# Kernel optimization log

Hardware: AMD Instinct MI355X
Metric: run time of the kernel (lower is better)

The kernel has to match this reference:

```python
import jax, jax.numpy as jnp
import numpy as np

B, S, D, H = 256, 128, 1024, 8
DH = D // H  # per-head dim = input_length / head


def setup_inputs() -> dict:
    key = jax.random.key(0)
    ks = jax.random.split(key, 12)
    code = jax.random.normal(ks[0], (B, S, D), dtype=jnp.float32)
    # 0/1 adjacency (PDG relation mask)
    input_relation = jax.random.bernoulli(ks[1], 0.2, (B, S, S)).astype(jnp.float32)
    w = 0.02
    Wq = jax.random.normal(ks[2], (H, D, DH), dtype=jnp.float32) * w
    bq = jnp.zeros((H, DH), dtype=jnp.float32)
    Wk = jax.random.normal(ks[3], (H, D, DH), dtype=jnp.float32) * w
    bk = jnp.zeros((H, DH), dtype=jnp.float32)
    Wv = jax.random.normal(ks[4], (H, D, DH), dtype=jnp.float32) * w
    bv = jnp.zeros((H, DH), dtype=jnp.float32)
    Wo = jax.random.normal(ks[5], (2 * D, D), dtype=jnp.float32) * w
    bo = jnp.zeros((D,), dtype=jnp.float32)
    return {"code": code, "input_relation": input_relation,
            "Wq": Wq, "bq": bq, "Wk": Wk, "bk": bk,
            "Wv": Wv, "bv": bv, "Wo": Wo, "bo": bo}


def reference(code, input_relation, Wq, bq, Wk, bk, Wv, bv, Wo, bo):
    Hn = Wq.shape[0]
    half = Hn // 2
    Sn = code.shape[1]
    E = jnp.eye(Sn, dtype=code.dtype)
    # Faithful to the TF loop: head i < H/2 sees relation + i*I (the loop
    # reassigns input_relation = this_relation + I each iteration);
    # heads i >= H/2 see the ORIGINAL transposed relation.
    i_idx = jnp.arange(half, dtype=code.dtype)  # [half]
    rel_fwd = input_relation[None] + i_idx[:, None, None, None] * E  # [half,B,S,S]
    rel_t = jnp.swapaxes(input_relation, 1, 2)
    rel_bwd = jnp.broadcast_to(rel_t[None], (Hn - half,) + rel_t.shape)
    rels = jnp.concatenate([rel_fwd, rel_bwd], axis=0)  # [H,B,S,S]

    relu = jax.nn.relu
    Q = relu(jnp.einsum('bsd,hdf->hbsf', code, Wq) + bq[:, None, None, :])
    K = relu(jnp.einsum('bsd,hdf->hbsf', code, Wk) + bk[:, None, None, :])
    V = relu(jnp.einsum('bsd,hdf->hbsf', code, Wv) + bv[:, None, None, :])

    attn = jnp.einsum('hbsf,hbtf->hbst', Q, K)  # [H,B,S,S]
    pdg = rels * attn + 1e-11
    # tf.reduce_sum axis=1 (rows) -> our axis=2; axis=2 (cols) -> our axis=3
    indeg = jnp.sqrt(jnp.sum(pdg, axis=2, keepdims=True))   # [H,B,1,S]
    outdeg = jnp.sqrt(jnp.sum(pdg, axis=3, keepdims=True))  # [H,B,S,1]
    pdg = pdg / indeg / outdeg
    softed = rels * pdg
    res = jnp.einsum('hbst,hbtf->hbsf', softed, V)  # [H,B,S,DH]

    # concat heads along features (head 0 first), then concat original code
    all_ch = jnp.transpose(res, (1, 2, 0, 3)).reshape(code.shape[0], Sn, -1)
    add_ori = jnp.concatenate([all_ch, code], axis=-1)  # [B,S,2D]
    out = relu(add_ori @ Wo + bo)
    return out
```

## Files before the change

kernel.cpp:

```cpp
#include <hip/hip_runtime.h>
#include <cstdint>
#include <cstddef>

#define B_  256
#define S_  128
#define D_  1024
#define H_  8
#define DH_ 128
#define M_  (B_ * S_)

typedef _Float16 half8 __attribute__((ext_vector_type(8)));
typedef float    f32x4 __attribute__((ext_vector_type(4)));

#define GLOAD_LDS16(gp, lp)                                                    \
    __builtin_amdgcn_global_load_lds(                                          \
        (const __attribute__((address_space(1))) void*)(gp),                   \
        (__attribute__((address_space(3))) void*)(lp), 16, 0, 0)

__global__ __launch_bounds__(256)
void cvt_code(const float* __restrict__ src, _Float16* __restrict__ dst, int n8)
{
    int i = blockIdx.x * 256 + threadIdx.x;
    if (i >= n8) return;
    const float4* s = (const float4*)src;
    float4 a = s[2 * i], b = s[2 * i + 1];
    half8 o;
    o[0] = (_Float16)a.x; o[1] = (_Float16)a.y; o[2] = (_Float16)a.z; o[3] = (_Float16)a.w;
    o[4] = (_Float16)b.x; o[5] = (_Float16)b.y; o[6] = (_Float16)b.z; o[7] = (_Float16)b.w;
    *(half8*)(dst + (size_t)i * 8) = o;
}

__global__ __launch_bounds__(256)
void cvt_wqkv(const float* __restrict__ Wq, const float* __restrict__ Wk,
              const float* __restrict__ Wv,
              const float* __restrict__ bq, const float* __restrict__ bk,
              const float* __restrict__ bv,
              _Float16* __restrict__ Wt, float* __restrict__ bias_all)
{
    int idx = blockIdx.x * 256 + threadIdx.x;
    if (idx >= 3072 * 128) return;
    int n = idx >> 7, kc = idx & 127, k = kc * 8;
    int qkv = n >> 10, hf = n & 1023, h = hf >> 7, f = hf & 127;
    const float* W = (qkv == 0 ? Wq : (qkv == 1 ? Wk : Wv))
                     + (size_t)h * D_ * DH_ + (size_t)k * DH_ + f;
    half8 o;
    #pragma unroll
    for (int j = 0; j < 8; ++j) o[j] = (_Float16)W[(size_t)j * DH_];
    *(half8*)(Wt + (size_t)n * 1024 + k) = o;
    if (kc == 0)
        bias_all[n] = (qkv == 0 ? bq : (qkv == 1 ? bk : bv))[h * DH_ + f];
}

__global__ __launch_bounds__(256)
void cvt_wo(const float* __restrict__ Wo, _Float16* __restrict__ Wot)
{
    int idx = blockIdx.x * 256 + threadIdx.x;
    if (idx >= 1024 * 256) return;
    int n = idx >> 8, kc = idx & 255, k = kc * 8;
    const float* W = Wo + (size_t)k * 1024 + n;
    half8 o;
    #pragma unroll
    for (int j = 0; j < 8; ++j) o[j] = (_Float16)W[(size_t)j * 1024];
    *(half8*)(Wot + (size_t)n * 2048 + k) = o;
}

template <bool OUTF32>
__global__ __launch_bounds__(512, 4)
void gemm_f16_b32(const _Float16* __restrict__ A1p, const _Float16* __restrict__ A2p,
                  int K1, const _Float16* __restrict__ Bt,
                  const float* __restrict__ bias, void* __restrict__ outp,
                  int Ntot, int Ktot, int ntn)
{
    __shared__ __align__(16) char lds[49152];

    const int tid = threadIdx.x;
    const int w = tid >> 6, l = tid & 63;
    const int wm = w >> 2, wn = w & 3;
    const int lr = l & 15, lg = l >> 4;

    const int cpx = gridDim.x >> 3;
    const int bid = blockIdx.x;
    const int swz = (bid & 7) * cpx + (bid >> 3);
    const int m0 = (swz / ntn) * 128, n0 = (swz % ntn) * 256;

    const int NT = Ktot >> 5;

    auto stage = [&](int bufi, int t) {
        const int k0 = t << 5;
        char* base = lds + bufi * 24576;
        const int rr = l >> 2, cc = (l & 3) * 8;
        {
            const _Float16* Asrc; int kc;
            if (k0 < K1) { Asrc = A1p; kc = k0; } else { Asrc = A2p; kc = k0 - K1; }
            const _Float16* g = Asrc + (size_t)(m0 + w * 16 + rr) * 1024 + kc + cc;
            GLOAD_LDS16(g, base + w * 1024);
        }
        #pragma unroll
        for (int i = 0; i < 2; ++i) {
            const int row = i * 128 + w * 16 + rr;
            const _Float16* g = Bt + (size_t)(n0 + row) * Ktot + k0 + cc;
            GLOAD_LDS16(g, base + 8192 + i * 8192 + w * 1024);
        }
    };

    f32x4 acc[4][4] = {};

    stage(0, 0);

    for (int t = 0; t < NT; ++t) {
        const int buf = t & 1;
        const bool nl = (t + 1 < NT);

        asm volatile("s_waitcnt vmcnt(0)" ::: "memory");
        __builtin_amdgcn_s_barrier();

        if (nl) stage(buf ^ 1, t + 1);

        half8 af[4], bf[4];
        #pragma unroll
        for (int i = 0; i < 4; ++i)
            af[i] = *(const half8*)(lds + buf * 24576 + (wm * 64 + i * 16 + lr) * 64 + lg * 16);
        #pragma unroll
        for (int j = 0; j < 4; ++j)
            bf[j] = *(const half8*)(lds + buf * 24576 + 8192 + (wn * 64 + j * 16 + lr) * 64 + lg * 16);

        __builtin_amdgcn_s_setprio(1);
        #pragma unroll
        for (int i = 0; i < 4; ++i)
            #pragma unroll
            for (int j = 0; j < 4; ++j)
                acc[i][j] = __builtin_amdgcn_mfma_f32_16x16x32_f16(
                    af[i], bf[j], acc[i][j], 0, 0, 0);
        __builtin_amdgcn_s_setprio(0);
    }

    #pragma unroll
    for (int i = 0; i < 4; ++i) {
        #pragma unroll
        for (int j = 0; j < 4; ++j) {
            const int n = n0 + wn * 64 + j * 16 + lr;
            const float bs = bias[n];
            #pragma unroll
            for (int rg = 0; rg < 4; ++rg) {
                const int m = m0 + wm * 64 + i * 16 + lg * 4 + rg;
                float v = acc[i][j][rg] + bs;
                v = v > 0.0f ? v : 0.0f;
                if constexpr (OUTF32)
                    ((float*)outp)[(size_t)m * Ntot + n] = v;
                else
                    ((_Float16*)outp)[(size_t)m * Ntot + n] = (_Float16)v;
            }
        }
    }
}

__global__ __launch_bounds__(256, 2)
void attn_pdg_mfma(const _Float16* __restrict__ QKV, const float* __restrict__ Rel,
                   _Float16* __restrict__ resh)
{
    __shared__ __align__(16) char smem[75776];
    unsigned* rbits = (unsigned*)(smem + 70656);
    float* rowpart  = (float*)(smem + 72704);
    float* colpart  = (float*)(smem + 73728);
    float* inv_in   = (float*)(smem + 74752);
    float* inv_out  = (float*)(smem + 75264);

    const int tid = threadIdx.x;
    const int w = tid >> 6, l = tid & 63;
    const int wr = w >> 1, wc = w & 1;
    const int lr = l & 15, lg = l >> 4;
    const int h = blockIdx.x, b = blockIdx.y;

    for (int s = w; s < S_; s += 4) {
        const float* row = &Rel[((size_t)b * S_ + s) * S_];
        unsigned long long b0m = __ballot(row[l] > 0.5f);
        unsigned long long b1m = __ballot(row[64 + l] > 0.5f);
        if (l == 0) {
            rbits[s * 4 + 0] = (unsigned)b0m; rbits[s * 4 + 1] = (unsigned)(b0m >> 32);
            rbits[s * 4 + 2] = (unsigned)b1m; rbits[s * 4 + 3] = (unsigned)(b1m >> 32);
        }
    }

    const size_t gbase = (size_t)(b * S_) * 3072 + h * DH_;

    const _Float16* Vb = QKV + gbase + 2048;
    const int vrow = tid >> 1, vcol0 = (tid & 1) * 64;
    uint4 vreg[8];
    #pragma unroll
    for (int j = 0; j < 8; ++j)
        vreg[j] = *(const uint4*)&Vb[(size_t)vrow * 3072 + vcol0 + j * 8];

    #pragma unroll
    for (int i = 0; i < 8; ++i) {
        const int row = (w * 8 + i) * 4 + (l >> 4);
        const int gsrc = (l & 15) ^ (row & 7);
        const _Float16* gq = QKV + gbase + (size_t)row * 3072 + gsrc * 8;
        GLOAD_LDS16(gq, smem + (w * 8 + i) * 1024);
        const _Float16* gk = QKV + gbase + 1024 + (size_t)row * 3072 + gsrc * 8;
        GLOAD_LDS16(gk, smem + 32768 + (w * 8 + i) * 1024);
    }
    __syncthreads();

    f32x4 acc[4][4] = {};
    #pragma unroll
    for (int kc = 0; kc < 4; ++kc) {
        half8 af[4], bf[4];
        #pragma unroll
        for (int i = 0; i < 4; ++i) {
            const int row = wr * 64 + i * 16 + lr;
            const int pos = (kc * 4 + lg) ^ (row & 7);
            af[i] = *(const half8*)(smem + row * 256 + pos * 16);
        }
        #pragma unroll
        for (int j = 0; j < 4; ++j) {
            const int row = wc * 64 + j * 16 + lr;
            const int pos = (kc * 4 + lg) ^ (row & 7);
            bf[j] = *(const half8*)(smem + 32768 + row * 256 + pos * 16);
        }
        #pragma unroll
        for (int i = 0; i < 4; ++i)
            #pragma unroll
            for (int j = 0; j < 4; ++j)
                acc[i][j] = __builtin_amdgcn_mfma_f32_16x16x32_f16(af[i], bf[j], acc[i][j], 0, 0, 0);
    }

    auto relf = [&](int s, int t) -> float {
        float r;
        if (h < H_ / 2) {
            r = (float)((rbits[s * 4 + (t >> 5)] >> (t & 31)) & 1u);
            if (s == t) r += (float)h;
        } else {
            r = (float)((rbits[t * 4 + (s >> 5)] >> (s & 31)) & 1u);
        }
        return r;
    };

    f32x4 p[4][4];
    #pragma unroll
    for (int i = 0; i < 4; ++i)
        #pragma unroll
        for (int j = 0; j < 4; ++j)
            #pragma unroll
            for (int rg = 0; rg < 4; ++rg) {
                const int s = wr * 64 + i * 16 + lg * 4 + rg;
                const int t = wc * 64 + j * 16 + lr;
                p[i][j][rg] = relf(s, t) * acc[i][j][rg] + 1e-11f;
            }

    #pragma unroll
    for (int i = 0; i < 4; ++i)
        #pragma unroll
        for (int rg = 0; rg < 4; ++rg) {
            float part = p[i][0][rg] + p[i][1][rg] + p[i][2][rg] + p[i][3][rg];
            part += __shfl_xor(part, 1);
            part += __shfl_xor(part, 2);
            part += __shfl_xor(part, 4);
            part += __shfl_xor(part, 8);
            if (lr == 0) rowpart[wc * 128 + wr * 64 + i * 16 + lg * 4 + rg] = part;
        }
    #pragma unroll
    for (int j = 0; j < 4; ++j) {
        float part = 0.0f;
        #pragma unroll
        for (int i = 0; i < 4; ++i)
            part += p[i][j][0] + p[i][j][1] + p[i][j][2] + p[i][j][3];
        part += __shfl_xor(part, 16);
        part += __shfl_xor(part, 32);
        if (lg == 0) colpart[wr * 128 + wc * 64 + j * 16 + lr] = part;
    }
    __syncthreads();

    if (tid < 128) {
        inv_in[tid] = rsqrtf(colpart[tid] + colpart[128 + tid]);
    } else {
        const int s = tid - 128;
        inv_out[s] = rsqrtf(rowpart[s] + rowpart[128 + s]);
    }
    __syncthreads();

    float itj[4];
    #pragma unroll
    for (int j = 0; j < 4; ++j) itj[j] = inv_in[wc * 64 + j * 16 + lr];
    #pragma unroll
    for (int i = 0; i < 4; ++i)
        #pragma unroll
        for (int rg = 0; rg < 4; ++rg) {
            const int s = wr * 64 + i * 16 + lg * 4 + rg;
            const float os = inv_out[s];
            #pragma unroll
            for (int j = 0; j < 4; ++j) {
                const int t = wc * 64 + j * 16 + lr;
                const float val = relf(s, t) * p[i][j][rg] * itj[j] * os;
                *(_Float16*)(smem + s * 272 + t * 2) = (_Float16)val;
            }
        }

    #pragma unroll
    for (int j = 0; j < 8; ++j) {
        union { uint4 u; _Float16 hh[8]; } uu;
        uu.u = vreg[j];
        #pragma unroll
        for (int e = 0; e < 8; ++e) {
            const int f = vcol0 + j * 8 + e;
            *(_Float16*)(smem + 34816 + f * 280 + vrow * 2) = uu.hh[e];
        }
    }
    __syncthreads();

    f32x4 acc2[4][4] = {};
    #pragma unroll
    for (int kc = 0; kc < 4; ++kc) {
        half8 af[4], bf[4];
        #pragma unroll
        for (int i = 0; i < 4; ++i)
            af[i] = *(const half8*)(smem + (wr * 64 + i * 16 + lr) * 272 + kc * 64 + lg * 16);
        #pragma unroll
        for (int j = 0; j < 4; ++j)
            bf[j] = *(const half8*)(smem + 34816 + (wc * 64 + j * 16 + lr) * 280 + kc * 64 + lg * 16);
        #pragma unroll
        for (int i = 0; i < 4; ++i)
            #pragma unroll
            for (int j = 0; j < 4; ++j)
                acc2[i][j] = __builtin_amdgcn_mfma_f32_16x16x32_f16(af[i], bf[j], acc2[i][j], 0, 0, 0);
    }

    #pragma unroll
    for (int i = 0; i < 4; ++i)
        #pragma unroll
        for (int rg = 0; rg < 4; ++rg) {
            const int s = wr * 64 + i * 16 + lg * 4 + rg;
            #pragma unroll
            for (int j = 0; j < 4; ++j) {
                const int f = wc * 64 + j * 16 + lr;
                resh[((size_t)(b * S_ + s)) * 1024 + h * DH_ + f] = (_Float16)acc2[i][j][rg];
            }
        }
}

extern "C" void kernel_launch(void* const* d_in, const int* in_sizes, int n_in,
                              void* d_out, int out_size, void* d_ws, size_t ws_size,
                              hipStream_t stream)
{
    const float* code = (const float*)d_in[0];
    const float* Rel  = (const float*)d_in[1];
    const float* Wq   = (const float*)d_in[2];
    const float* bq   = (const float*)d_in[3];
    const float* Wk   = (const float*)d_in[4];
    const float* bk   = (const float*)d_in[5];
    const float* Wv   = (const float*)d_in[6];
    const float* bv   = (const float*)d_in[7];
    const float* Wo   = (const float*)d_in[8];
    const float* bo   = (const float*)d_in[9];
    float* out = (float*)d_out;
    (void)in_sizes; (void)n_in; (void)out_size; (void)ws_size;

    char* wsp = (char*)d_ws;
    _Float16* codeh = (_Float16*)wsp;  wsp += (size_t)M_ * 1024 * 2;
    _Float16* QKV   = (_Float16*)wsp;  wsp += (size_t)M_ * 3072 * 2;
    _Float16* resh  = (_Float16*)wsp;  wsp += (size_t)M_ * 1024 * 2;
    _Float16* Wt    = (_Float16*)wsp;  wsp += (size_t)3072 * 1024 * 2;
    _Float16* Wot   = (_Float16*)wsp;  wsp += (size_t)1024 * 2048 * 2;
    float* bias_all = (float*)wsp;     wsp += 3072 * 4;

    cvt_code<<<(M_ * 1024 / 8 + 255) / 256, 256, 0, stream>>>(code, codeh, M_ * 1024 / 8);
    cvt_wqkv<<<(3072 * 128 + 255) / 256, 256, 0, stream>>>(Wq, Wk, Wv, bq, bk, bv, Wt, bias_all);
    cvt_wo<<<(1024 * 256 + 255) / 256, 256, 0, stream>>>(Wo, Wot);

    gemm_f16_b32<false><<<(M_ / 128) * (3072 / 256), 512, 0, stream>>>(
        codeh, codeh, 1024, Wt, bias_all, (void*)QKV, 3072, 1024, 3072 / 256);

    attn_pdg_mfma<<<dim3(H_, B_), 256, 0, stream>>>(QKV, Rel, resh);

    gemm_f16_b32<true><<<(M_ / 128) * (1024 / 256), 512, 0, stream>>>(
        resh, codeh, 1024, Wot, bo, (void*)out, 1024, 2048, 1024 / 256);
}
```

Before: 620.8 us.

## Use 4-wave GEMM with 64x128 per-wave tiles and XOR-swizzled LDS layout

The two projection GEMMs now launch 256-thread blocks instead of 512, keeping the same 128x256 block tile. Each wave computes a 64x128 sub-tile with 32 accumulators, so every A fragment is reused across 8 B fragments. LDS rows are XOR-swizzled on the 16-byte chunk index, both on the global-to-LDS copy and on the fragment reads, to cut bank conflicts. In exchange, register pressure per thread roughly doubles and the launch bound drops to 2 blocks per CU, which may reduce latency hiding.

Measured after the change: 623.4 us. Within noise of the previous version (+0.4%).

```diff
diff --git a/kernel.cpp b/kernel.cpp
--- a/kernel.cpp
+++ b/kernel.cpp
@@ -65,17 +65,17 @@
 }
 
 template <bool OUTF32>
-__global__ __launch_bounds__(512, 4)
-void gemm_f16_b32(const _Float16* __restrict__ A1p, const _Float16* __restrict__ A2p,
-                  int K1, const _Float16* __restrict__ Bt,
-                  const float* __restrict__ bias, void* __restrict__ outp,
-                  int Ntot, int Ktot, int ntn)
+__global__ __launch_bounds__(256, 2)
+void gemm_f16_w128(const _Float16* __restrict__ A1p, const _Float16* __restrict__ A2p,
+                   int K1, const _Float16* __restrict__ Bt,
+                   const float* __restrict__ bias, void* __restrict__ outp,
+                   int Ntot, int Ktot, int ntn)
 {
     __shared__ __align__(16) char lds[49152];
 
     const int tid = threadIdx.x;
     const int w = tid >> 6, l = tid & 63;
-    const int wm = w >> 2, wn = w & 3;
+    const int wm = w >> 1, wn = w & 1;
     const int lr = l & 15, lg = l >> 4;
 
     const int cpx = gridDim.x >> 3;
@@ -85,25 +85,45 @@
 
     const int NT = Ktot >> 5;
 
+    const int rr = l >> 2, gl = l & 3;
+
     auto stage = [&](int bufi, int t) {
         const int k0 = t << 5;
         char* base = lds + bufi * 24576;
-        const int rr = l >> 2, cc = (l & 3) * 8;
         {
             const _Float16* Asrc; int kc;
             if (k0 < K1) { Asrc = A1p; kc = k0; } else { Asrc = A2p; kc = k0 - K1; }
-            const _Float16* g = Asrc + (size_t)(m0 + w * 16 + rr) * 1024 + kc + cc;
-            GLOAD_LDS16(g, base + w * 1024);
-        }
-        #pragma unroll
-        for (int i = 0; i < 2; ++i) {
-            const int row = i * 128 + w * 16 + rr;
-            const _Float16* g = Bt + (size_t)(n0 + row) * Ktot + k0 + cc;
-            GLOAD_LDS16(g, base + 8192 + i * 8192 + w * 1024);
+            #pragma unroll
+            for (int i = 0; i < 2; ++i) {
+                const int c = i * 4 + w;
+                const int row = c * 16 + rr;
+                const int gcol = (gl ^ ((row >> 1) & 3)) * 8;
+                const _Float16* g = Asrc + (size_t)(m0 + row) * 1024 + kc + gcol;
+                GLOAD_LDS16(g, base + c * 1024);
+            }
+        }
+        #pragma unroll
+        for (int i = 0; i < 4; ++i) {
+            const int c = i * 4 + w;
+            const int row = c * 16 + rr;
+            const int gcol = (gl ^ ((row >> 1) & 3)) * 8;
+            const _Float16* g = Bt + (size_t)(n0 + row) * Ktot + k0 + gcol;
+            GLOAD_LDS16(g, base + 8192 + c * 1024);
         }
     };
 
-    f32x4 acc[4][4] = {};
+    auto ldA = [&](int bufi, int fi) -> half8 {
+        const int row = wm * 64 + fi * 16 + lr;
+        const int pos = lg ^ ((row >> 1) & 3);
+        return *(const half8*)(lds + bufi * 24576 + row * 64 + pos * 16);
+    };
+    auto ldB = [&](int bufi, int fj) -> half8 {
+        const int row = wn * 128 + fj * 16 + lr;
+        const int pos = lg ^ ((row >> 1) & 3);
+        return *(const half8*)(lds + bufi * 24576 + 8192 + row * 64 + pos * 16);
+    };
+
+    f32x4 acc[4][8] = {};
 
     stage(0, 0);
 
@@ -116,19 +136,17 @@
 
         if (nl) stage(buf ^ 1, t + 1);
 
-        half8 af[4], bf[4];
-        #pragma unroll
-        for (int i = 0; i < 4; ++i)
-            af[i] = *(const half8*)(lds + buf * 24576 + (wm * 64 + i * 16 + lr) * 64 + lg * 16);
-        #pragma unroll
-        for (int j = 0; j < 4; ++j)
-            bf[j] = *(const half8*)(lds + buf * 24576 + 8192 + (wn * 64 + j * 16 + lr) * 64 + lg * 16);
+        half8 af[4], bf[8];
+        #pragma unroll
+        for (int i = 0; i < 4; ++i) af[i] = ldA(buf, i);
+        #pragma unroll
+        for (int j = 0; j < 8; ++j) bf[j] = ldB(buf, j);
 
         __builtin_amdgcn_s_setprio(1);
         #pragma unroll
         for (int i = 0; i < 4; ++i)
             #pragma unroll
-            for (int j = 0; j < 4; ++j)
+            for (int j = 0; j < 8; ++j)
                 acc[i][j] = __builtin_amdgcn_mfma_f32_16x16x32_f16(
                     af[i], bf[j], acc[i][j], 0, 0, 0);
         __builtin_amdgcn_s_setprio(0);
@@ -137,8 +155,8 @@
     #pragma unroll
     for (int i = 0; i < 4; ++i) {
         #pragma unroll
-        for (int j = 0; j < 4; ++j) {
-            const int n = n0 + wn * 64 + j * 16 + lr;
+        for (int j = 0; j < 8; ++j) {
+            const int n = n0 + wn * 128 + j * 16 + lr;
             const float bs = bias[n];
             #pragma unroll
             for (int rg = 0; rg < 4; ++rg) {
@@ -366,11 +384,11 @@
     cvt_wqkv<<<(3072 * 128 + 255) / 256, 256, 0, stream>>>(Wq, Wk, Wv, bq, bk, bv, Wt, bias_all);
     cvt_wo<<<(1024 * 256 + 255) / 256, 256, 0, stream>>>(Wo, Wot);
 
-    gemm_f16_b32<false><<<(M_ / 128) * (3072 / 256), 512, 0, stream>>>(
+    gemm_f16_w128<false><<<(M_ / 128) * (3072 / 256), 256, 0, stream>>>(
         codeh, codeh, 1024, Wt, bias_all, (void*)QKV, 3072, 1024, 3072 / 256);
 
     attn_pdg_mfma<<<dim3(H_, B_), 256, 0, stream>>>(QKV, Rel, resh);
 
-    gemm_f16_b32<true><<<(M_ / 128) * (1024 / 256), 512, 0, stream>>>(
+    gemm_f16_w128<true><<<(M_ / 128) * (1024 / 256), 256, 0, stream>>>(
         resh, codeh, 1024, Wot, bo, (void*)out, 1024, 2048, 1024 / 256);
 }
```

## Rewrite GEMM as 256x256 tile with 8-phase pipelined chunk staging

Applied to the files above, without the earlier changes.

Replaces the 128x256 double-buffered GEMM with a 256x256 tile and a K-step of 64. The LDS layout is XOR-swizzled, and the K-loop is split into eight phases that interleave quarter-tile global-to-LDS loads with MFMA blocks under explicit barriers and priority hints. The goal is to raise arithmetic intensity per LDS byte, avoid bank conflicts, and overlap memory traffic with compute. The cost is 128KB of LDS and 128 accumulator registers per lane, which limits the kernel to one block per CU.

Measured after the change: 584.2 us. 5.9% less time.

```diff
diff --git a/kernel.cpp b/kernel.cpp
--- a/kernel.cpp
+++ b/kernel.cpp
@@ -65,13 +65,13 @@
 }
 
 template <bool OUTF32>
-__global__ __launch_bounds__(512, 4)
-void gemm_f16_b32(const _Float16* __restrict__ A1p, const _Float16* __restrict__ A2p,
-                  int K1, const _Float16* __restrict__ Bt,
-                  const float* __restrict__ bias, void* __restrict__ outp,
-                  int Ntot, int Ktot, int ntn)
-{
-    __shared__ __align__(16) char lds[49152];
+__global__ __launch_bounds__(512, 1)
+void gemm_f16_8p(const _Float16* __restrict__ A1p, const _Float16* __restrict__ A2p,
+                 int K1, const _Float16* __restrict__ Bt,
+                 const float* __restrict__ bias, void* __restrict__ outp,
+                 int Ntot, int Ktot, int ntn)
+{
+    __shared__ __align__(16) char lds[131072];
 
     const int tid = threadIdx.x;
     const int w = tid >> 6, l = tid & 63;
@@ -81,69 +81,144 @@
     const int cpx = gridDim.x >> 3;
     const int bid = blockIdx.x;
     const int swz = (bid & 7) * cpx + (bid >> 3);
-    const int m0 = (swz / ntn) * 128, n0 = (swz % ntn) * 256;
-
-    const int NT = Ktot >> 5;
-
-    auto stage = [&](int bufi, int t) {
-        const int k0 = t << 5;
-        char* base = lds + bufi * 24576;
-        const int rr = l >> 2, cc = (l & 3) * 8;
-        {
+    const int m0 = (swz / ntn) * 256, n0 = (swz % ntn) * 256;
+
+    const int NT = Ktot >> 6;
+    const int NI = NT >> 1;
+
+    const int srow8 = l >> 3;
+    const int gsw   = ((l & 7) ^ srow8) * 8;
+
+    auto stageChunk = [&](int bufi, int t, int chunk) {
+        const int k0 = t << 6;
+        if (chunk == 0 || chunk == 2) {
             const _Float16* Asrc; int kc;
             if (k0 < K1) { Asrc = A1p; kc = k0; } else { Asrc = A2p; kc = k0 - K1; }
-            const _Float16* g = Asrc + (size_t)(m0 + w * 16 + rr) * 1024 + kc + cc;
-            GLOAD_LDS16(g, base + w * 1024);
-        }
-        #pragma unroll
-        for (int i = 0; i < 2; ++i) {
-            const int row = i * 128 + w * 16 + rr;
-            const _Float16* g = Bt + (size_t)(n0 + row) * Ktot + k0 + cc;
-            GLOAD_LDS16(g, base + 8192 + i * 8192 + w * 1024);
+            char* dbase = lds + bufi * 65536 + (chunk == 2 ? 16384 : 0);
+            const int soff = (chunk == 2 ? 128 : 0);
+            #pragma unroll
+            for (int i = 0; i < 2; ++i) {
+                const int c = i * 8 + w;
+                const int s = soff + c * 8 + srow8;
+                const int srow = (s & 63) | (((s >> 6) & 1) << 7) | (((s >> 7) & 1) << 6);
+                const _Float16* g = Asrc + (size_t)(m0 + srow) * 1024 + kc + gsw;
+                GLOAD_LDS16(g, dbase + c * 1024);
+            }
+        } else {
+            char* dbase = lds + bufi * 65536 + 32768 + (chunk == 1 ? 16384 : 0);
+            const int soff = (chunk == 1 ? 128 : 0);
+            #pragma unroll
+            for (int i = 0; i < 2; ++i) {
+                const int c = i * 8 + w;
+                const int s = soff + c * 8 + srow8;
+                const int srow = (s & 31) | (((s >> 5) & 3) << 6) | (((s >> 7) & 1) << 5);
+                const _Float16* g = Bt + (size_t)(n0 + srow) * Ktot + k0 + gsw;
+                GLOAD_LDS16(g, dbase + c * 1024);
+            }
         }
     };
 
-    f32x4 acc[4][4] = {};
-
-    stage(0, 0);
-
-    for (int t = 0; t < NT; ++t) {
-        const int buf = t & 1;
-        const bool nl = (t + 1 < NT);
-
-        asm volatile("s_waitcnt vmcnt(0)" ::: "memory");
-        __builtin_amdgcn_s_barrier();
-
-        if (nl) stage(buf ^ 1, t + 1);
-
-        half8 af[4], bf[4];
-        #pragma unroll
-        for (int i = 0; i < 4; ++i)
-            af[i] = *(const half8*)(lds + buf * 24576 + (wm * 64 + i * 16 + lr) * 64 + lg * 16);
-        #pragma unroll
-        for (int j = 0; j < 4; ++j)
-            bf[j] = *(const half8*)(lds + buf * 24576 + 8192 + (wn * 64 + j * 16 + lr) * 64 + lg * 16);
-
-        __builtin_amdgcn_s_setprio(1);
-        #pragma unroll
-        for (int i = 0; i < 4; ++i)
-            #pragma unroll
-            for (int j = 0; j < 4; ++j)
-                acc[i][j] = __builtin_amdgcn_mfma_f32_16x16x32_f16(
-                    af[i], bf[j], acc[i][j], 0, 0, 0);
-        __builtin_amdgcn_s_setprio(0);
-    }
-
-    #pragma unroll
-    for (int i = 0; i < 4; ++i) {
-        #pragma unroll
-        for (int j = 0; j < 4; ++j) {
-            const int n = n0 + wn * 64 + j * 16 + lr;
+    half8 aq[4][2], b0[2][2], b1[2][2];
+    f32x4 acc[8][4] = {};
+
+    auto rdA = [&](int bufi, int qm) {
+        #pragma unroll
+        for (int f = 0; f < 4; ++f)
+            #pragma unroll
+            for (int ks = 0; ks < 2; ++ks) {
+                const int slot = qm * 128 + wm * 64 + f * 16 + lr;
+                const int pos = (ks * 4 + lg) ^ (lr & 7);
+                aq[f][ks] = *(const half8*)(lds + bufi * 65536 + slot * 128 + pos * 16);
+            }
+    };
+    auto rdB = [&](half8 bb[2][2], int bufi, int qn) {
+        #pragma unroll
+        for (int f = 0; f < 2; ++f)
+            #pragma unroll
+            for (int ks = 0; ks < 2; ++ks) {
+                const int slot = qn * 128 + wn * 32 + f * 16 + lr;
+                const int pos = (ks * 4 + lg) ^ (lr & 7);
+                bb[f][ks] = *(const half8*)(lds + bufi * 65536 + 32768 + slot * 128 + pos * 16);
+            }
+    };
+    auto mm16 = [&](half8 bb[2][2], int qm, int qn) {
+        #pragma unroll
+        for (int ks = 0; ks < 2; ++ks)
+            #pragma unroll
+            for (int f = 0; f < 4; ++f)
+                #pragma unroll
+                for (int j = 0; j < 2; ++j)
+                    acc[qm * 4 + f][qn * 2 + j] = __builtin_amdgcn_mfma_f32_16x16x32_f16(
+                        aq[f][ks], bb[j][ks], acc[qm * 4 + f][qn * 2 + j], 0, 0, 0);
+    };
+
+#define PHASE_TAIL()                                              \
+    __builtin_amdgcn_s_barrier();                                 \
+    asm volatile("s_waitcnt lgkmcnt(0)" ::: "memory");            \
+    __builtin_amdgcn_sched_barrier(0);                            \
+    __builtin_amdgcn_s_setprio(1)
+
+#define PHASE_END()                                               \
+    __builtin_amdgcn_s_setprio(0);                                \
+    __builtin_amdgcn_s_barrier();                                 \
+    __builtin_amdgcn_sched_barrier(0)
+
+    stageChunk(0, 0, 0); stageChunk(0, 0, 1); stageChunk(0, 0, 2); stageChunk(0, 0, 3);
+    stageChunk(1, 1, 0); stageChunk(1, 1, 1); stageChunk(1, 1, 2);
+    asm volatile("s_waitcnt vmcnt(6)" ::: "memory");
+    __builtin_amdgcn_s_barrier();
+    __builtin_amdgcn_sched_barrier(0);
+
+    for (int I = 0; I < NI; ++I) {
+        const int u = 2 * I;
+        const bool nl = (I + 1 < NI);
+
+        rdA(0, 0); rdB(b0, 0, 0);
+        stageChunk(1, u + 1, 3);
+        PHASE_TAIL(); mm16(b0, 0, 0); PHASE_END();
+        rdB(b1, 0, 1);
+        if (nl) stageChunk(0, u + 2, 0);
+        PHASE_TAIL(); mm16(b1, 0, 1); PHASE_END();
+        rdA(0, 1);
+        if (nl) stageChunk(0, u + 2, 1);
+        PHASE_TAIL(); mm16(b1, 1, 1); PHASE_END();
+        rdB(b0, 0, 0);
+        if (nl) {
+            stageChunk(0, u + 2, 2);
+            asm volatile("s_waitcnt vmcnt(6)" ::: "memory");
+        } else {
+            asm volatile("s_waitcnt vmcnt(0)" ::: "memory");
+        }
+        PHASE_TAIL(); mm16(b0, 1, 0); PHASE_END();
+        rdA(1, 0); rdB(b0, 1, 0);
+        if (nl) stageChunk(0, u + 2, 3);
+        PHASE_TAIL(); mm16(b0, 0, 0); PHASE_END();
+        rdB(b1, 1, 1);
+        if (nl) stageChunk(1, u + 3, 0);
+        PHASE_TAIL(); mm16(b1, 0, 1); PHASE_END();
+        rdA(1, 1);
+        if (nl) stageChunk(1, u + 3, 1);
+        PHASE_TAIL(); mm16(b1, 1, 1); PHASE_END();
+        rdB(b0, 1, 0);
+        if (nl) {
+            stageChunk(1, u + 3, 2);
+            asm volatile("s_waitcnt vmcnt(6)" ::: "memory");
+        }
+        PHASE_TAIL(); mm16(b0, 1, 0); PHASE_END();
+    }
+#undef PHASE_TAIL
+#undef PHASE_END
+
+    #pragma unroll
+    for (int fi = 0; fi < 8; ++fi) {
+        #pragma unroll
+        for (int fj = 0; fj < 4; ++fj) {
+            const int n = n0 + wn * 64 + fj * 16 + lr;
             const float bs = bias[n];
             #pragma unroll
             for (int rg = 0; rg < 4; ++rg) {
-                const int m = m0 + wm * 64 + i * 16 + lg * 4 + rg;
-                float v = acc[i][j][rg] + bs;
+                const int m = m0 + wm * 128 + fi * 16 + lg * 4 + rg;
+                float v = acc[fi][fj][rg] + bs;
                 v = v > 0.0f ? v : 0.0f;
                 if constexpr (OUTF32)
                     ((float*)outp)[(size_t)m * Ntot + n] = v;
@@ -366,11 +441,11 @@
     cvt_wqkv<<<(3072 * 128 + 255) / 256, 256, 0, stream>>>(Wq, Wk, Wv, bq, bk, bv, Wt, bias_all);
     cvt_wo<<<(1024 * 256 + 255) / 256, 256, 0, stream>>>(Wo, Wot);
 
-    gemm_f16_b32<false><<<(M_ / 128) * (3072 / 256), 512, 0, stream>>>(
+    gemm_f16_8p<false><<<(M_ / 256) * (3072 / 256), 512, 0, stream>>>(
         codeh, codeh, 1024, Wt, bias_all, (void*)QKV, 3072, 1024, 3072 / 256);
 
     attn_pdg_mfma<<<dim3(H_, B_), 256, 0, stream>>>(QKV, Rel, resh);
 
-    gemm_f16_b32<true><<<(M_ / 128) * (1024 / 256), 512, 0, stream>>>(
+    gemm_f16_8p<true><<<(M_ / 256) * (1024 / 256), 512, 0, stream>>>(
         resh, codeh, 1024, Wot, bo, (void*)out, 1024, 2048, 1024 / 256);
 }
```
